# Optimization experiments

Hardware: AMD Instinct MI355X
Metric: run time of the kernel (lower is better)

The kernel has to match this reference:

```python
import jax, jax.numpy as jnp
import numpy as np

N_HEADS = 16


def setup_inputs() -> dict:
    key = jax.random.key(0)
    k_x, k_len, k_pos, k_attn, k_proj = jax.random.split(key, 5)
    B, W, c, C = 4, 256, 32, 1024
    x = jax.random.normal(k_x, (B, W, c, C), dtype=jnp.float32)
    # ragged word lengths in [1, c]; left-aligned padding mask as in pad()
    lengths = jax.random.randint(k_len, (B, W), 1, c + 1)
    attention_mask = (jnp.arange(c)[None, None, :] < lengths[:, :, None]).astype(jnp.int32)
    pos_emb = jax.random.normal(k_pos, (W, C), dtype=jnp.float32) * 0.02
    attn_w = jax.random.normal(k_attn, (C, 3 * C), dtype=jnp.float32) * (C ** -0.5)
    proj_w = jax.random.normal(k_proj, (C, C), dtype=jnp.float32) * (C ** -0.5)
    return {"x": x, "attention_mask": attention_mask, "pos_emb": pos_emb,
            "attn_w": attn_w, "proj_w": proj_w}


def reference(x, attention_mask, pos_emb, attn_w, proj_w):
    # first_time=True path of CharAttention.forward (eval mode: dropout = identity)
    B, W, c, C = x.shape
    H = N_HEADS
    hd = C // H
    last_ix = jnp.sum(attention_mask, axis=2) - 1          # [B, W]

    qkv = jnp.einsum('bwce,ef->bwcf', x, attn_w)            # [B, W, c, 3C]
    q, k, v = jnp.split(qkv, 3, axis=-1)
    # [B, W, c, C] -> [B, W, H, c, hd]
    def to_heads(t):
        return t.reshape(B, W, c, H, hd).transpose(0, 1, 3, 2, 4)
    q, k, v = to_heads(q), to_heads(k), to_heads(v)

    scale = 1.0 / jnp.sqrt(jnp.asarray(hd, dtype=x.dtype))
    scores = jnp.einsum('bwhqd,bwhkd->bwhqk', q, k) * scale  # [B, W, H, c, c]
    causal = jnp.tril(jnp.ones((c, c), dtype=bool))
    scores = jnp.where(causal[None, None, None], scores, jnp.finfo(x.dtype).min)
    attn = jax.nn.softmax(scores, axis=-1)
    o = jnp.einsum('bwhqk,bwhkd->bwhqd', attn, v)            # [B, W, H, c, hd]
    o = o.transpose(0, 1, 3, 2, 4).reshape(B, W, c, C)       # [B, W, c, C]

    # gather the last real-character position of each word
    idx = last_ix[:, :, None, None]                          # [B, W, 1, 1]
    gathered = jnp.take_along_axis(o, idx, axis=2)[:, :, 0, :]  # [B, W, C]

    out = gathered + pos_emb[None, :, :]
    out = jnp.einsum('bwe,ef->bwf', out, proj_w)
    return out
```

## Files before the change

kernel.cpp:

```cpp
#include <hip/hip_runtime.h>
#include <hip/hip_bf16.h>
#include <stdint.h>

typedef __attribute__((ext_vector_type(8))) short short8;
typedef __attribute__((ext_vector_type(4))) float floatx4;

#define GPTR(p) (const __attribute__((address_space(1))) void*)(p)
#define LPTR(p) (__attribute__((address_space(3))) void*)(p)

__device__ __forceinline__ ushort f2bf(float f) {
    union { float f; uint32_t u; } v; v.f = f;
    uint32_t u = v.u;
    uint32_t r = (u + 0x7FFFu + ((u >> 16) & 1u)) >> 16;
    return (ushort)r;
}
__device__ __forceinline__ float bf2f(ushort b) {
    union { uint32_t u; float f; } v; v.u = ((uint32_t)b) << 16;
    return v.f;
}

__global__ void prep_kernel(const float* __restrict__ attn_w, const float* __restrict__ proj_w,
                            const float* __restrict__ x, const int* __restrict__ mask,
                            ushort* __restrict__ wqT, ushort* __restrict__ wk,
                            ushort* __restrict__ wvT, ushort* __restrict__ wpT,
                            ushort* __restrict__ xq) {
    __shared__ float tile[32][33];
    __shared__ int t_sh;
    const int bx = blockIdx.x, by = blockIdx.y;
    const int tid = threadIdx.x;

    if (bx >= 128) {
        int bw = (bx - 128) * 32 + by;
        if (tid < 32) {
            int s = mask[bw * 32 + tid];
            #pragma unroll
            for (int off = 16; off; off >>= 1) s += __shfl_xor(s, off);
            if (tid == 0) t_sh = s - 1;
        }
        __syncthreads();
        int t = t_sh;
        float4 v = ((const float4*)(x + ((size_t)bw * 32 + t) * 1024))[tid];
        ushort4 o;
        o.x = f2bf(v.x); o.y = f2bf(v.y); o.z = f2bf(v.z); o.w = f2bf(v.w);
        ((ushort4*)(xq + (size_t)bw * 1024))[tid] = o;
        return;
    }

    const int tx = tid & 31, ty = tid >> 5;
    const int r0 = by * 32;
    if (bx >= 96) {
        int c0 = (bx - 96) * 32;
        for (int i = ty; i < 32; i += 8)
            wk[(size_t)(r0 + i) * 1024 + c0 + tx] =
                f2bf(attn_w[(size_t)(r0 + i) * 3072 + 1024 + c0 + tx]);
        return;
    }
    const float* src; ushort* dst; int N, csrc0, c0;
    if (bx < 32)      { src = attn_w; dst = wqT; N = 3072; c0 = bx * 32;        csrc0 = c0; }
    else if (bx < 64) { src = attn_w; dst = wvT; N = 3072; c0 = (bx - 32) * 32; csrc0 = 2048 + c0; }
    else              { src = proj_w; dst = wpT; N = 1024; c0 = (bx - 64) * 32; csrc0 = c0; }
    for (int i = ty; i < 32; i += 8)
        tile[i][tx] = src[(size_t)(r0 + i) * N + csrc0 + tx];
    __syncthreads();
    for (int i = ty; i < 32; i += 8)
        dst[(size_t)(c0 + i) * 1024 + r0 + tx] = f2bf(tile[tx][i]);
}

__global__ __launch_bounds__(256)
void gemm64sk_kernel(const ushort* __restrict__ A, const ushort* __restrict__ Bt,
                     float* __restrict__ Cpart) {
    __shared__ ushort As[64 * 32];
    __shared__ ushort Bs[64 * 32];

    const int bm = blockIdx.x, bn = blockIdx.y, z = blockIdx.z;
    const int kofs = z * 256;

    const int tid  = threadIdx.x;
    const int wave = tid >> 6;
    const int lane = tid & 63;
    const int wm = wave & 1, wn = wave >> 1;
    const int quad = lane >> 4, l15 = lane & 15;

    floatx4 acc[2][2] = {};

    const int srow = wave * 16 + (lane >> 2);
    const int kcol = (lane & 3) * 8;

    for (int kt = 0; kt < 256; kt += 32) {
        const ushort* gA = A  + (size_t)(bm * 64 + srow) * 1024 + kofs + kt + kcol;
        const ushort* gB = Bt + (size_t)(bn * 64 + srow) * 1024 + kofs + kt + kcol;
        ushort* lA = As + (wave * 16) * 32;
        ushort* lB = Bs + (wave * 16) * 32;
        __builtin_amdgcn_global_load_lds(GPTR(gA), LPTR(lA), 16, 0, 0);
        __builtin_amdgcn_global_load_lds(GPTR(gB), LPTR(lB), 16, 0, 0);
        __syncthreads();

        short8 af[2], bf[2];
        #pragma unroll
        for (int i = 0; i < 2; ++i)
            af[i] = *(const short8*)&As[(wm * 32 + i * 16 + l15) * 32 + quad * 8];
        #pragma unroll
        for (int j = 0; j < 2; ++j)
            bf[j] = *(const short8*)&Bs[(wn * 32 + j * 16 + l15) * 32 + quad * 8];
        #pragma unroll
        for (int i = 0; i < 2; ++i)
            #pragma unroll
            for (int j = 0; j < 2; ++j)
                acc[i][j] = __builtin_amdgcn_mfma_f32_16x16x32_bf16(af[i], bf[j], acc[i][j], 0, 0, 0);
        __syncthreads();
    }

    #pragma unroll
    for (int i = 0; i < 2; ++i) {
        #pragma unroll
        for (int j = 0; j < 2; ++j) {
            int r0 = bm * 64 + wm * 32 + i * 16 + quad * 4;
            int c  = bn * 64 + wn * 32 + j * 16 + l15;
            #pragma unroll
            for (int r = 0; r < 4; ++r)
                Cpart[(size_t)z * 1048576 + (size_t)(r0 + r) * 1024 + c] = acc[i][j][r];
        }
    }
}

template <bool OUT_BF16>
__global__ void combine4_kernel(const float* __restrict__ P, void* __restrict__ C) {
    int i = blockIdx.x * 256 + threadIdx.x;
    const float4* p = (const float4*)P;
    float4 a = p[i], b = p[i + 262144], c = p[i + 524288], d = p[i + 786432];
    float4 s;
    s.x = a.x + b.x + c.x + d.x;
    s.y = a.y + b.y + c.y + d.y;
    s.z = a.z + b.z + c.z + d.z;
    s.w = a.w + b.w + c.w + d.w;
    if (OUT_BF16) {
        ushort4 o;
        o.x = f2bf(s.x); o.y = f2bf(s.y); o.z = f2bf(s.z); o.w = f2bf(s.w);
        ((ushort4*)C)[i] = o;
    } else {
        ((float4*)C)[i] = s;
    }
}

__global__ __launch_bounds__(256)
void gemmu_kernel(const ushort* __restrict__ A, const ushort* __restrict__ Bt,
                  ushort* __restrict__ C) {
    const int bm = blockIdx.x, bn = blockIdx.y, z = blockIdx.z;
    const int tid  = threadIdx.x;
    const int wave = tid >> 6;
    const int lane = tid & 63;
    const int wm = wave & 1, wn = wave >> 1;
    const int quad = lane >> 4, l15 = lane & 15;

    const ushort* Ab = A  + (size_t)(bm * 128 + wm * 64 + l15) * 1024 + z * 64 + quad * 8;
    const ushort* Bb = Bt + (size_t)(bn * 128 + wn * 64 + l15) * 1024 + z * 64 + quad * 8;

    short8 af[4][2], bfr[4][2];
    #pragma unroll
    for (int i = 0; i < 4; ++i)
        #pragma unroll
        for (int kk = 0; kk < 2; ++kk) {
            af[i][kk]  = *(const short8*)(Ab + (size_t)(i * 16) * 1024 + kk * 32);
            bfr[i][kk] = *(const short8*)(Bb + (size_t)(i * 16) * 1024 + kk * 32);
        }

    floatx4 acc[4][4] = {};
    #pragma unroll
    for (int kk = 0; kk < 2; ++kk)
        #pragma unroll
        for (int i = 0; i < 4; ++i)
            #pragma unroll
            for (int j = 0; j < 4; ++j)
                acc[i][j] = __builtin_amdgcn_mfma_f32_16x16x32_bf16(af[i][kk], bfr[j][kk], acc[i][j], 0, 0, 0);

    #pragma unroll
    for (int i = 0; i < 4; ++i) {
        #pragma unroll
        for (int j = 0; j < 4; ++j) {
            int r0 = bm * 128 + wm * 64 + i * 16 + quad * 4;
            int c  = bn * 128 + wn * 64 + j * 16 + l15;
            #pragma unroll
            for (int r = 0; r < 4; ++r)
                C[(size_t)(r0 + r) * 16384 + (size_t)z * 1024 + c] = f2bf(acc[i][j][r]);
        }
    }
}

template <bool OUT_BF16, bool ADD_POS>
__global__ __launch_bounds__(256)
void gemm64_kernel(const ushort* __restrict__ A, int lda, long sA,
                   const ushort* __restrict__ Bt, int ldb, long sB,
                   void* __restrict__ C, int ldc, int cColPerZ, int K,
                   const float* __restrict__ pos) {
    __shared__ ushort As[64 * 32];
    __shared__ ushort Bs[64 * 32];

    const int bm = blockIdx.x, bn = blockIdx.y, z = blockIdx.z;
    A  += (size_t)z * sA;
    Bt += (size_t)z * sB;

    const int tid  = threadIdx.x;
    const int wave = tid >> 6;
    const int lane = tid & 63;
    const int wm = wave & 1, wn = wave >> 1;
    const int quad = lane >> 4, l15 = lane & 15;

    floatx4 acc[2][2] = {};

    const int srow = wave * 16 + (lane >> 2);
    const int kcol = (lane & 3) * 8;

    for (int kt = 0; kt < K; kt += 32) {
        const ushort* gA = A  + (size_t)(bm * 64 + srow) * lda + kt + kcol;
        const ushort* gB = Bt + (size_t)(bn * 64 + srow) * ldb + kt + kcol;
        ushort* lA = As + (wave * 16) * 32;
        ushort* lB = Bs + (wave * 16) * 32;
        __builtin_amdgcn_global_load_lds(GPTR(gA), LPTR(lA), 16, 0, 0);
        __builtin_amdgcn_global_load_lds(GPTR(gB), LPTR(lB), 16, 0, 0);
        __syncthreads();

        short8 af[2], bf[2];
        #pragma unroll
        for (int i = 0; i < 2; ++i)
            af[i] = *(const short8*)&As[(wm * 32 + i * 16 + l15) * 32 + quad * 8];
        #pragma unroll
        for (int j = 0; j < 2; ++j)
            bf[j] = *(const short8*)&Bs[(wn * 32 + j * 16 + l15) * 32 + quad * 8];
        #pragma unroll
        for (int i = 0; i < 2; ++i)
            #pragma unroll
            for (int j = 0; j < 2; ++j)
                acc[i][j] = __builtin_amdgcn_mfma_f32_16x16x32_bf16(af[i], bf[j], acc[i][j], 0, 0, 0);
        __syncthreads();
    }

    #pragma unroll
    for (int i = 0; i < 2; ++i) {
        #pragma unroll
        for (int j = 0; j < 2; ++j) {
            int r0 = bm * 64 + wm * 32 + i * 16 + quad * 4;
            int cc = z * cColPerZ + bn * 64 + wn * 32 + j * 16 + l15;
            #pragma unroll
            for (int r = 0; r < 4; ++r) {
                float v = acc[i][j][r];
                if (ADD_POS) v += pos[(size_t)((r0 + r) & 255) * 1024 + cc];
                size_t idx = (size_t)(r0 + r) * ldc + cc;
                if (OUT_BF16) ((ushort*)C)[idx] = f2bf(v);
                else          ((float*) C)[idx] = v;
            }
        }
    }
}

__global__ __launch_bounds__(256)
void attn2_kernel(const float* __restrict__ x, const int* __restrict__ mask,
                  const ushort* __restrict__ U, ushort* __restrict__ Z) {
    __shared__ float  Sp[2][16][16];
    __shared__ float  Ss[16 * 36];
    __shared__ float  Ps[32 * 16];
    __shared__ int    t_sh;

    const int bw = blockIdx.x;
    const int tid = threadIdx.x;
    const int wave = tid >> 6, lane = tid & 63;
    const int quad = lane >> 4, l15 = lane & 15;

    if (tid < 32) {
        int s = mask[bw * 32 + tid];
        #pragma unroll
        for (int off = 16; off; off >>= 1) s += __shfl_xor(s, off);
        if (tid == 0) t_sh = s - 1;
    }
    __syncthreads();
    const int t = t_sh;

    const int m  = wave & 1;
    const int kh = wave >> 1;
    const int row = m * 16 + l15;
    const bool live = (row <= t);

    const float*  xrow = x + ((size_t)bw * 32 + row) * 1024 + kh * 512 + quad * 8;
    const ushort* urow = U + (size_t)bw * 16384 + (size_t)l15 * 1024 + kh * 512 + quad * 8;

    floatx4 acc = {0.f, 0.f, 0.f, 0.f};
    #pragma unroll
    for (int ks = 0; ks < 16; ++ks) {
        short8 a = (short8)0;
        if (live) {
            float4 v0 = *(const float4*)(xrow + ks * 32);
            float4 v1 = *(const float4*)(xrow + ks * 32 + 4);
            a[0] = (short)f2bf(v0.x); a[1] = (short)f2bf(v0.y);
            a[2] = (short)f2bf(v0.z); a[3] = (short)f2bf(v0.w);
            a[4] = (short)f2bf(v1.x); a[5] = (short)f2bf(v1.y);
            a[6] = (short)f2bf(v1.z); a[7] = (short)f2bf(v1.w);
        }
        short8 b = *(const short8*)(urow + ks * 32);
        acc = __builtin_amdgcn_mfma_f32_16x16x32_bf16(a, b, acc, 0, 0, 0);
    }

    if (kh == 1) {
        #pragma unroll
        for (int r = 0; r < 4; ++r) Sp[m][quad * 4 + r][l15] = acc[r];
    }
    __syncthreads();
    if (kh == 0) {
        #pragma unroll
        for (int r = 0; r < 4; ++r)
            Ss[l15 * 36 + m * 16 + quad * 4 + r] =
                (acc[r] + Sp[m][quad * 4 + r][l15]) * 0.125f;
    }
    __syncthreads();

    if (wave == 0) {
        float s[8]; float mx = -1e30f;
        #pragma unroll
        for (int r = 0; r < 8; ++r) {
            int j = quad * 8 + r;
            float v = Ss[l15 * 36 + j];
            v = (j <= t) ? v : -1e30f;
            s[r] = v; mx = fmaxf(mx, v);
        }
        mx = fmaxf(mx, __shfl_xor(mx, 16));
        mx = fmaxf(mx, __shfl_xor(mx, 32));
        float l = 0.f;
        #pragma unroll
        for (int r = 0; r < 8; ++r) { s[r] = __expf(s[r] - mx); l += s[r]; }
        l += __shfl_xor(l, 16);
        l += __shfl_xor(l, 32);
        float inv = 1.f / l;
        #pragma unroll
        for (int r = 0; r < 8; ++r)
            Ps[(quad * 8 + r) * 16 + l15] = s[r] * inv;
    }
    __syncthreads();

    const float4* xsrc = (const float4*)(x + (size_t)bw * 32768);
    float z[16][4];
    #pragma unroll
    for (int h = 0; h < 16; ++h)
        #pragma unroll
        for (int cc = 0; cc < 4; ++cc) z[h][cc] = 0.f;
    for (int j = 0; j <= t; ++j) {
        float4 p0 = *(const float4*)&Ps[j * 16 + 0];
        float4 p1 = *(const float4*)&Ps[j * 16 + 4];
        float4 p2 = *(const float4*)&Ps[j * 16 + 8];
        float4 p3 = *(const float4*)&Ps[j * 16 + 12];
        float pr[16] = {p0.x, p0.y, p0.z, p0.w, p1.x, p1.y, p1.z, p1.w,
                        p2.x, p2.y, p2.z, p2.w, p3.x, p3.y, p3.z, p3.w};
        float4 xv = xsrc[j * 256 + tid];
        float xf[4] = {xv.x, xv.y, xv.z, xv.w};
        #pragma unroll
        for (int h = 0; h < 16; ++h)
            #pragma unroll
            for (int cc = 0; cc < 4; ++cc)
                z[h][cc] += pr[h] * xf[cc];
    }
    const int e0 = tid * 4;
    #pragma unroll
    for (int h = 0; h < 16; ++h) {
        ushort4 o;
        o.x = f2bf(z[h][0]); o.y = f2bf(z[h][1]);
        o.z = f2bf(z[h][2]); o.w = f2bf(z[h][3]);
        *(ushort4*)&Z[(size_t)bw * 16384 + h * 1024 + e0] = o;
    }
}

extern "C" void kernel_launch(void* const* d_in, const int* in_sizes, int n_in,
                              void* d_out, int out_size, void* d_ws, size_t ws_size,
                              hipStream_t stream) {
    const float* x        = (const float*)d_in[0];
    const int*   mask     = (const int*)  d_in[1];
    const float* pos_emb  = (const float*)d_in[2];
    const float* attn_w   = (const float*)d_in[3];
    const float* proj_w   = (const float*)d_in[4];
    float*       out      = (float*)d_out;

    const long MB2 = 1048576;

    char* ws = (char*)d_ws;
    size_t off = 0;
    ushort* U_bf  = (ushort*)(ws + off); off += (size_t)16 * MB2 * 2;
    ushort* Z_bf  = (ushort*)(ws + off); off += (size_t)16 * MB2 * 2;
    float*  qpart = (float*) (ws + off); off += (size_t)4 * MB2 * 4;
    float*  opart = (float*) (ws + off); off += (size_t)4 * MB2 * 4;
    ushort* wqT   = (ushort*)(ws + off); off += MB2 * 2;
    ushort* wk    = (ushort*)(ws + off); off += MB2 * 2;
    ushort* wvT   = (ushort*)(ws + off); off += MB2 * 2;
    ushort* wpT   = (ushort*)(ws + off); off += MB2 * 2;
    ushort* xq_bf = (ushort*)(ws + off); off += MB2 * 2;
    ushort* q_bf  = (ushort*)(ws + off); off += MB2 * 2;
    ushort* y_bf  = (ushort*)(ws + off); off += MB2 * 2;

    prep_kernel<<<dim3(160, 32), 256, 0, stream>>>(attn_w, proj_w, x, mask,
                                                   wqT, wk, wvT, wpT, xq_bf);

    gemm64sk_kernel<<<dim3(16, 16, 4), 256, 0, stream>>>(xq_bf, wqT, qpart);
    combine4_kernel<true><<<1024, 256, 0, stream>>>(qpart, (void*)q_bf);

    gemmu_kernel<<<dim3(8, 8, 16), 256, 0, stream>>>(q_bf, wk, U_bf);

    attn2_kernel<<<1024, 256, 0, stream>>>(x, mask, U_bf, Z_bf);

    gemm64_kernel<true, true><<<dim3(16, 1, 16), 256, 0, stream>>>(
        Z_bf, 16384, 1024, wvT, 1024, 65536, (void*)y_bf, 1024, 64, 1024, pos_emb);

    gemm64sk_kernel<<<dim3(16, 16, 4), 256, 0, stream>>>(y_bf, wpT, opart);
    combine4_kernel<false><<<1024, 256, 0, stream>>>(opart, (void*)out);
}
```

Before: 276.5 us.

## Double-buffer LDS in GEMM kernel and drop split-K with combine passes

Replaces the split-K GEMM plus combine kernels and the single-buffered batched GEMM with one double-buffered GEMM kernel. It prefetches the next K tile into a second LDS buffer while MFMAs run on the current one, and it computes full K per block. This removes the partial-sum writes and reads, the two combine launches, and one barrier per K step. In exchange the projection GEMMs now launch only 256 blocks instead of 1024, which lowers parallelism, and LDS use per block doubles.

```diff
diff --git a/kernel.cpp b/kernel.cpp
--- a/kernel.cpp
+++ b/kernel.cpp
@@ -66,14 +66,18 @@
         dst[(size_t)(c0 + i) * 1024 + r0 + tx] = f2bf(tile[tx][i]);
 }
 
+template <bool OUT_BF16, bool ADD_POS>
 __global__ __launch_bounds__(256)
-void gemm64sk_kernel(const ushort* __restrict__ A, const ushort* __restrict__ Bt,
-                     float* __restrict__ Cpart) {
-    __shared__ ushort As[64 * 32];
-    __shared__ ushort Bs[64 * 32];
+void gemm64db_kernel(const ushort* __restrict__ A, int lda, long sA,
+                     const ushort* __restrict__ Bt, int ldb, long sB,
+                     void* __restrict__ C, int ldc, int cColPerZ, int K,
+                     const float* __restrict__ pos) {
+    __shared__ ushort As[2][64 * 32];
+    __shared__ ushort Bs[2][64 * 32];
 
     const int bm = blockIdx.x, bn = blockIdx.y, z = blockIdx.z;
-    const int kofs = z * 256;
+    A  += (size_t)z * sA;
+    Bt += (size_t)z * sB;
 
     const int tid  = threadIdx.x;
     const int wave = tid >> 6;
@@ -85,29 +89,34 @@
 
     const int srow = wave * 16 + (lane >> 2);
     const int kcol = (lane & 3) * 8;
-
-    for (int kt = 0; kt < 256; kt += 32) {
-        const ushort* gA = A  + (size_t)(bm * 64 + srow) * 1024 + kofs + kt + kcol;
-        const ushort* gB = Bt + (size_t)(bn * 64 + srow) * 1024 + kofs + kt + kcol;
-        ushort* lA = As + (wave * 16) * 32;
-        ushort* lB = Bs + (wave * 16) * 32;
-        __builtin_amdgcn_global_load_lds(GPTR(gA), LPTR(lA), 16, 0, 0);
-        __builtin_amdgcn_global_load_lds(GPTR(gB), LPTR(lB), 16, 0, 0);
-        __syncthreads();
-
+    const ushort* gA = A  + (size_t)(bm * 64 + srow) * lda + kcol;
+    const ushort* gB = Bt + (size_t)(bn * 64 + srow) * ldb + kcol;
+    const int lofs = wave * 512;
+
+    __builtin_amdgcn_global_load_lds(GPTR(gA), LPTR(As[0] + lofs), 16, 0, 0);
+    __builtin_amdgcn_global_load_lds(GPTR(gB), LPTR(Bs[0] + lofs), 16, 0, 0);
+    __syncthreads();
+
+    int cur = 0;
+    for (int kt = 0; kt < K; kt += 32) {
+        if (kt + 32 < K) {
+            __builtin_amdgcn_global_load_lds(GPTR(gA + kt + 32), LPTR(As[cur ^ 1] + lofs), 16, 0, 0);
+            __builtin_amdgcn_global_load_lds(GPTR(gB + kt + 32), LPTR(Bs[cur ^ 1] + lofs), 16, 0, 0);
+        }
         short8 af[2], bf[2];
         #pragma unroll
         for (int i = 0; i < 2; ++i)
-            af[i] = *(const short8*)&As[(wm * 32 + i * 16 + l15) * 32 + quad * 8];
+            af[i] = *(const short8*)&As[cur][(wm * 32 + i * 16 + l15) * 32 + quad * 8];
         #pragma unroll
         for (int j = 0; j < 2; ++j)
-            bf[j] = *(const short8*)&Bs[(wn * 32 + j * 16 + l15) * 32 + quad * 8];
+            bf[j] = *(const short8*)&Bs[cur][(wn * 32 + j * 16 + l15) * 32 + quad * 8];
         #pragma unroll
         for (int i = 0; i < 2; ++i)
             #pragma unroll
             for (int j = 0; j < 2; ++j)
                 acc[i][j] = __builtin_amdgcn_mfma_f32_16x16x32_bf16(af[i], bf[j], acc[i][j], 0, 0, 0);
         __syncthreads();
+        cur ^= 1;
     }
 
     #pragma unroll
@@ -115,30 +124,16 @@
         #pragma unroll
         for (int j = 0; j < 2; ++j) {
             int r0 = bm * 64 + wm * 32 + i * 16 + quad * 4;
-            int c  = bn * 64 + wn * 32 + j * 16 + l15;
-            #pragma unroll
-            for (int r = 0; r < 4; ++r)
-                Cpart[(size_t)z * 1048576 + (size_t)(r0 + r) * 1024 + c] = acc[i][j][r];
-        }
-    }
-}
-
-template <bool OUT_BF16>
-__global__ void combine4_kernel(const float* __restrict__ P, void* __restrict__ C) {
-    int i = blockIdx.x * 256 + threadIdx.x;
-    const float4* p = (const float4*)P;
-    float4 a = p[i], b = p[i + 262144], c = p[i + 524288], d = p[i + 786432];
-    float4 s;
-    s.x = a.x + b.x + c.x + d.x;
-    s.y = a.y + b.y + c.y + d.y;
-    s.z = a.z + b.z + c.z + d.z;
-    s.w = a.w + b.w + c.w + d.w;
-    if (OUT_BF16) {
-        ushort4 o;
-        o.x = f2bf(s.x); o.y = f2bf(s.y); o.z = f2bf(s.z); o.w = f2bf(s.w);
-        ((ushort4*)C)[i] = o;
-    } else {
-        ((float4*)C)[i] = s;
+            int cc = z * cColPerZ + bn * 64 + wn * 32 + j * 16 + l15;
+            #pragma unroll
+            for (int r = 0; r < 4; ++r) {
+                float v = acc[i][j][r];
+                if (ADD_POS) v += pos[(size_t)((r0 + r) & 255) * 1024 + cc];
+                size_t idx = (size_t)(r0 + r) * ldc + cc;
+                if (OUT_BF16) ((ushort*)C)[idx] = f2bf(v);
+                else          ((float*) C)[idx] = v;
+            }
+        }
     }
 }
 
@@ -182,72 +177,6 @@
             #pragma unroll
             for (int r = 0; r < 4; ++r)
                 C[(size_t)(r0 + r) * 16384 + (size_t)z * 1024 + c] = f2bf(acc[i][j][r]);
-        }
-    }
-}
-
-template <bool OUT_BF16, bool ADD_POS>
-__global__ __launch_bounds__(256)
-void gemm64_kernel(const ushort* __restrict__ A, int lda, long sA,
-                   const ushort* __restrict__ Bt, int ldb, long sB,
-                   void* __restrict__ C, int ldc, int cColPerZ, int K,
-                   const float* __restrict__ pos) {
-    __shared__ ushort As[64 * 32];
-    __shared__ ushort Bs[64 * 32];
-
-    const int bm = blockIdx.x, bn = blockIdx.y, z = blockIdx.z;
-    A  += (size_t)z * sA;
-    Bt += (size_t)z * sB;
-
-    const int tid  = threadIdx.x;
-    const int wave = tid >> 6;
-    const int lane = tid & 63;
-    const int wm = wave & 1, wn = wave >> 1;
-    const int quad = lane >> 4, l15 = lane & 15;
-
-    floatx4 acc[2][2] = {};
-
-    const int srow = wave * 16 + (lane >> 2);
-    const int kcol = (lane & 3) * 8;
-
-    for (int kt = 0; kt < K; kt += 32) {
-        const ushort* gA = A  + (size_t)(bm * 64 + srow) * lda + kt + kcol;
-        const ushort* gB = Bt + (size_t)(bn * 64 + srow) * ldb + kt + kcol;
-        ushort* lA = As + (wave * 16) * 32;
-        ushort* lB = Bs + (wave * 16) * 32;
-        __builtin_amdgcn_global_load_lds(GPTR(gA), LPTR(lA), 16, 0, 0);
-        __builtin_amdgcn_global_load_lds(GPTR(gB), LPTR(lB), 16, 0, 0);
-        __syncthreads();
-
-        short8 af[2], bf[2];
-        #pragma unroll
-        for (int i = 0; i < 2; ++i)
-            af[i] = *(const short8*)&As[(wm * 32 + i * 16 + l15) * 32 + quad * 8];
-        #pragma unroll
-        for (int j = 0; j < 2; ++j)
-            bf[j] = *(const short8*)&Bs[(wn * 32 + j * 16 + l15) * 32 + quad * 8];
-        #pragma unroll
-        for (int i = 0; i < 2; ++i)
-            #pragma unroll
-            for (int j = 0; j < 2; ++j)
-                acc[i][j] = __builtin_amdgcn_mfma_f32_16x16x32_bf16(af[i], bf[j], acc[i][j], 0, 0, 0);
-        __syncthreads();
-    }
-
-    #pragma unroll
-    for (int i = 0; i < 2; ++i) {
-        #pragma unroll
-        for (int j = 0; j < 2; ++j) {
-            int r0 = bm * 64 + wm * 32 + i * 16 + quad * 4;
-            int cc = z * cColPerZ + bn * 64 + wn * 32 + j * 16 + l15;
-            #pragma unroll
-            for (int r = 0; r < 4; ++r) {
-                float v = acc[i][j][r];
-                if (ADD_POS) v += pos[(size_t)((r0 + r) & 255) * 1024 + cc];
-                size_t idx = (size_t)(r0 + r) * ldc + cc;
-                if (OUT_BF16) ((ushort*)C)[idx] = f2bf(v);
-                else          ((float*) C)[idx] = v;
-            }
         }
     }
 }
@@ -381,8 +310,6 @@
     size_t off = 0;
     ushort* U_bf  = (ushort*)(ws + off); off += (size_t)16 * MB2 * 2;
     ushort* Z_bf  = (ushort*)(ws + off); off += (size_t)16 * MB2 * 2;
-    float*  qpart = (float*) (ws + off); off += (size_t)4 * MB2 * 4;
-    float*  opart = (float*) (ws + off); off += (size_t)4 * MB2 * 4;
     ushort* wqT   = (ushort*)(ws + off); off += MB2 * 2;
     ushort* wk    = (ushort*)(ws + off); off += MB2 * 2;
     ushort* wvT   = (ushort*)(ws + off); off += MB2 * 2;
@@ -394,16 +321,16 @@
     prep_kernel<<<dim3(160, 32), 256, 0, stream>>>(attn_w, proj_w, x, mask,
                                                    wqT, wk, wvT, wpT, xq_bf);
 
-    gemm64sk_kernel<<<dim3(16, 16, 4), 256, 0, stream>>>(xq_bf, wqT, qpart);
-    combine4_kernel<true><<<1024, 256, 0, stream>>>(qpart, (void*)q_bf);
+    gemm64db_kernel<true, false><<<dim3(16, 16, 1), 256, 0, stream>>>(
+        xq_bf, 1024, 0, wqT, 1024, 0, (void*)q_bf, 1024, 0, 1024, nullptr);
 
     gemmu_kernel<<<dim3(8, 8, 16), 256, 0, stream>>>(q_bf, wk, U_bf);
 
     attn2_kernel<<<1024, 256, 0, stream>>>(x, mask, U_bf, Z_bf);
 
-    gemm64_kernel<true, true><<<dim3(16, 1, 16), 256, 0, stream>>>(
+    gemm64db_kernel<true, true><<<dim3(16, 1, 16), 256, 0, stream>>>(
         Z_bf, 16384, 1024, wvT, 1024, 65536, (void*)y_bf, 1024, 64, 1024, pos_emb);
 
-    gemm64sk_kernel<<<dim3(16, 16, 4), 256, 0, stream>>>(y_bf, wpT, opart);
-    combine4_kernel<false><<<1024, 256, 0, stream>>>(opart, (void*)out);
-}
+    gemm64db_kernel<false, false><<<dim3(16, 16, 1), 256, 0, stream>>>(
+        y_bf, 1024, 0, wpT, 1024, 0, (void*)out, 1024, 0, 1024, nullptr);
+}
```

Measured after the change: 277.8 us. Within noise of the previous version (+0.5%).
